# Performance work log

Measured on AMD Instinct MI355X. Metric: run time of the kernel, lower is better.

## Reference

```python
import jax, jax.numpy as jnp
import numpy as np

DIL = (1, 2, 4)      # dilation_rates
SEG = (512, 512, 512)  # segment_sizes
H = 16               # num_heads
D = 1024             # d_model
B, L = 2, 8192


def _mha(x, Wqkv, bqkv, Wo, bo):
    # x: [..., S, D]; standard self-attention (FlashMHA math)
    lead = x.shape[:-2]
    S = x.shape[-2]
    hd = D // H
    qkv = x @ Wqkv.T + bqkv                      # [..., S, 3D]
    q, k, v = jnp.split(qkv, 3, axis=-1)
    q = q.reshape(*lead, S, H, hd)
    k = k.reshape(*lead, S, H, hd)
    v = v.reshape(*lead, S, H, hd)
    scale = 1.0 / np.float32(np.sqrt(hd))
    scores = jnp.einsum('...qhd,...khd->...hqk', q, k) * scale
    a = jax.nn.softmax(scores, axis=-1)
    o = jnp.einsum('...hqk,...khd->...qhd', a, v).reshape(*lead, S, D)
    return o @ Wo.T + bo


def setup_inputs() -> dict:
    key = jax.random.key(0)
    ks = jax.random.split(key, 5)
    n = len(DIL)
    x = jax.random.normal(ks[0], (B, L, D), dtype=jnp.float32)
    Wqkv = 0.02 * jax.random.normal(ks[1], (n, 3 * D, D), dtype=jnp.float32)
    bqkv = jnp.zeros((n, 3 * D), dtype=jnp.float32)
    Wout = 0.02 * jax.random.normal(ks[2], (n, D, D), dtype=jnp.float32)
    bout = jnp.zeros((n, D), dtype=jnp.float32)
    return {"x": x, "Wqkv": Wqkv, "bqkv": bqkv, "Wout": Wout, "bout": bout}


def reference(x, Wqkv, bqkv, Wout, bout):
    b_, L_, D_ = x.shape
    n = len(DIL)
    # Faithful to the original: zip(weights, all_head_outputs) truncates to the
    # first n = len(dilation_rates) of the (branch, offset) outputs.
    pairs = [(br, off) for br in range(n) for off in range(DIL[br])][:n]
    outs = []
    for br, off in pairs:
        r, S = DIL[br], SEG[br]
        xs = x[:, off::r, :].reshape(b_, -1, S, D_)   # [B, n_seg, S, D]
        att = _mha(xs, Wqkv[br], bqkv[br], Wout[br], bout[br])
        full = jnp.zeros_like(x).at[:, off::r, :].set(att.reshape(b_, -1, D_))
        outs.append(full)
    w = jax.nn.softmax(jnp.full((n,), 1.0 / n, dtype=x.dtype))  # uniform -> 1/n each
    res = outs[0] * w[0]
    for i in range(1, n):
        res = res + w[i] * outs[i]
    return res
```

## Files before the change

### kernel.cpp

```cpp
#include <hip/hip_runtime.h>
#include <math.h>

#define TOK    16384
#define DMODEL 1024
#define H3     3072
#define QKD    2048
#define LSEQ   8192
#define CHUNK  8192

typedef unsigned short ushort_t;
using bf16x8 = __attribute__((ext_vector_type(8))) __bf16;
using us8    = __attribute__((ext_vector_type(8))) unsigned short;
using f32x4  = __attribute__((ext_vector_type(4))) float;

__device__ __forceinline__ unsigned short f2bf(float f) {
    unsigned int u = __float_as_uint(f);
    u += 0x7FFF + ((u >> 16) & 1);
    return (unsigned short)(u >> 16);
}
__device__ __forceinline__ float bf2f(unsigned short b) {
    return __uint_as_float(((unsigned int)b) << 16);
}
__device__ __forceinline__ bf16x8 us8_to_bf(us8 u) {
    union { us8 u; bf16x8 b; } t; t.u = u; return t.b;
}

__device__ __forceinline__ void gld16(const void* g, void* l) {
    __builtin_amdgcn_global_load_lds(
        (const __attribute__((address_space(1))) unsigned int*)g,
        (__attribute__((address_space(3))) unsigned int*)l, 16, 0, 0);
}

__global__ __launch_bounds__(256) void split_f32(
    const float* __restrict__ s, ushort_t* __restrict__ h,
    ushort_t* __restrict__ l, int n4, int perm)
{
    int i = blockIdx.x * 256 + threadIdx.x;
    if (i >= n4) return;
    int src = i;
    if (perm) {
        int row = i >> 8, col = i & 255;
        int chunk = row >> 13, p = row & 8191;
        int orow = (chunk << 13) + ((p & 4095) * 2 + (p >> 12));
        src = orow * 256 + col;
    }
    float4 v = ((const float4*)s)[src];
    ushort4 hp, lp;
    hp.x = f2bf(v.x); lp.x = f2bf(v.x - bf2f(hp.x));
    hp.y = f2bf(v.y); lp.y = f2bf(v.y - bf2f(hp.y));
    hp.z = f2bf(v.z); lp.z = f2bf(v.z - bf2f(hp.z));
    hp.w = f2bf(v.w); lp.w = f2bf(v.w - bf2f(hp.w));
    ((ushort4*)h)[i] = hp;
    ((ushort4*)l)[i] = lp;
}

__global__ __launch_bounds__(256) void gemm_split_nt(
    const ushort_t* __restrict__ Ah, const ushort_t* __restrict__ Al,
    const ushort_t* __restrict__ Wh, const ushort_t* __restrict__ Wl,
    const float* __restrict__ bias, float* __restrict__ C,
    ushort_t* __restrict__ Ch, ushort_t* __restrict__ Cl,
    ushort_t* __restrict__ Vth, ushort_t* __restrict__ Vtl,
    int M, int N, int K, float scale, int beta, int qkv_mode)
{
    __shared__ __align__(16) ushort_t As[2][8 * 512];
    __shared__ __align__(16) ushort_t Bs[2][8 * 512];

    const int tid  = threadIdx.x;
    const int lane = tid & 63;
    const int w    = tid >> 6;
    const int m0 = blockIdx.y * 128;
    const int n0 = blockIdx.x * 128;

    const bool isA = (w < 2);
    const int  fb  = (w & 1) * 4;
    const int  blk0 = isA ? m0 : n0;
    long soff[4];
#pragma unroll
    for (int i = 0; i < 4; ++i) {
        int row = blk0 + (fb + i) * 16 + (lane & 15);
        soff[i] = (long)row * K + (lane >> 4) * 8;
    }
    ushort_t* dst_h = (isA ? As[0] : Bs[0]) + fb * 512;
    ushort_t* dst_l = (isA ? As[1] : Bs[1]) + fb * 512;
    const ushort_t* src_h = isA ? Ah : Wh;
    const ushort_t* src_l = isA ? Al : Wl;

    const int am0 = (w >> 1) * 4;
    const int bn0 = (w & 1) * 4;

    f32x4 acc[4][4];
#pragma unroll
    for (int i = 0; i < 4; ++i)
#pragma unroll
        for (int j = 0; j < 4; ++j) acc[i][j] = (f32x4){0.f, 0.f, 0.f, 0.f};

    for (int k0 = 0; k0 < K; k0 += 32) {
#pragma unroll
        for (int i = 0; i < 4; ++i) {
            gld16(src_h + soff[i] + k0, dst_h + i * 512);
            gld16(src_l + soff[i] + k0, dst_l + i * 512);
        }
        __syncthreads();

        bf16x8 ah[4], al[4], bh[4], bl[4];
#pragma unroll
        for (int i = 0; i < 4; ++i) {
            ah[i] = *(const bf16x8*)(As[0] + (am0 + i) * 512 + lane * 8);
            al[i] = *(const bf16x8*)(As[1] + (am0 + i) * 512 + lane * 8);
            bh[i] = *(const bf16x8*)(Bs[0] + (bn0 + i) * 512 + lane * 8);
            bl[i] = *(const bf16x8*)(Bs[1] + (bn0 + i) * 512 + lane * 8);
        }
#pragma unroll
        for (int i = 0; i < 4; ++i)
#pragma unroll
            for (int j = 0; j < 4; ++j)
                acc[i][j] = __builtin_amdgcn_mfma_f32_16x16x32_bf16(
                    ah[i], bh[j], acc[i][j], 0, 0, 0);
#pragma unroll
        for (int i = 0; i < 4; ++i)
#pragma unroll
            for (int j = 0; j < 4; ++j)
                acc[i][j] = __builtin_amdgcn_mfma_f32_16x16x32_bf16(
                    al[i], bh[j], acc[i][j], 0, 0, 0);
#pragma unroll
        for (int i = 0; i < 4; ++i)
#pragma unroll
            for (int j = 0; j < 4; ++j)
                acc[i][j] = __builtin_amdgcn_mfma_f32_16x16x32_bf16(
                    ah[i], bl[j], acc[i][j], 0, 0, 0);
        __syncthreads();
    }

    const int wm = (w >> 1) * 64, wn = (w & 1) * 64;
    const int r0 = (lane >> 4) * 4;
    const int cn = lane & 15;

    if (qkv_mode) {
        const bool isV = (n0 >= 1024 * 2);
#pragma unroll
        for (int j = 0; j < 4; ++j) {
            int col = n0 + wn + j * 16 + cn;
            float bv = bias[col];
#pragma unroll
            for (int i = 0; i < 4; ++i) {
                int rowb = m0 + wm + i * 16 + r0;
                if (isV) {
                    unsigned short ha[4], la[4];
#pragma unroll
                    for (int r = 0; r < 4; ++r) {
                        float v = acc[i][j][r] + bv;
                        ha[r] = f2bf(v);
                        la[r] = f2bf(v - bf2f(ha[r]));
                    }
                    size_t vidx = (size_t)(col - 2048) * M + rowb;
                    *(ushort4*)(Vth + vidx) = make_ushort4(ha[0], ha[1], ha[2], ha[3]);
                    *(ushort4*)(Vtl + vidx) = make_ushort4(la[0], la[1], la[2], la[3]);
                } else {
#pragma unroll
                    for (int r = 0; r < 4; ++r) {
                        float v = acc[i][j][r] + bv;
                        unsigned short hb = f2bf(v);
                        size_t idx = (size_t)(rowb + r) * QKD + col;
                        Ch[idx] = hb;
                        Cl[idx] = f2bf(v - bf2f(hb));
                    }
                }
            }
        }
    } else {
#pragma unroll
        for (int j = 0; j < 4; ++j) {
            int col = n0 + wn + j * 16 + cn;
            float bv = bias[col];
#pragma unroll
            for (int i = 0; i < 4; ++i) {
                int rowb = m0 + wm + i * 16 + r0;
#pragma unroll
                for (int r = 0; r < 4; ++r) {
                    size_t idx = (size_t)(rowb + r) * N + col;
                    float v = scale * (acc[i][j][r] + bv);
                    C[idx] = beta ? (C[idx] + v) : v;
                }
            }
        }
    }
}

__global__ __launch_bounds__(256) void attn_mfma(
    const ushort_t* __restrict__ qkh, const ushort_t* __restrict__ qkl,
    const ushort_t* __restrict__ vth, const ushort_t* __restrict__ vtl,
    ushort_t* __restrict__ aoh, ushort_t* __restrict__ aol,
    int perm, long tok0)
{
    __shared__ __align__(16) ushort_t Kls[2][4096];
    __shared__ __align__(16) ushort_t Vls[2][4096];
    __shared__ __align__(16) float    Ps[4][16 * 68];

    const int tid  = threadIdx.x;
    const int lane = tid & 63;
    const int w    = tid >> 6;
    const int l15  = lane & 15;
    const int lg   = lane >> 4;
    const int qt = blockIdx.x, h = blockIdx.y, z = blockIdx.z;
    const int base = z * 512;

    bf16x8 qh[2], ql[2];
    {
        const int qrow = base + qt * 64 + w * 16 + l15;
        const size_t rb = (size_t)qrow * QKD + h * 64 + lg * 8;
        qh[0] = *(const bf16x8*)(qkh + rb);
        ql[0] = *(const bf16x8*)(qkl + rb);
        qh[1] = *(const bf16x8*)(qkh + rb + 32);
        ql[1] = *(const bf16x8*)(qkl + rb + 32);
    }

    const bool isV = (w >> 1) != 0;
    const int  jm  = (w & 1) * 2;
    const ushort_t* srcH = isV ? vth : qkh;
    const ushort_t* srcL = isV ? vtl : qkl;
    size_t so[4];
    ushort_t *dH[4], *dL[4];
#pragma unroll
    for (int dj = 0; dj < 2; ++dj)
#pragma unroll
        for (int ks = 0; ks < 2; ++ks) {
            const int j = jm + dj, idx = dj * 2 + ks;
            if (!isV)
                so[idx] = (size_t)(base + 16 * j + l15) * QKD + 1024 + h * 64 + 32 * ks + lg * 8;
            else
                so[idx] = (size_t)(h * 64 + 16 * j + l15) * CHUNK + base + 32 * ks + lg * 8;
            dH[idx] = (isV ? Vls[0] : Kls[0]) + (j * 2 + ks) * 512;
            dL[idx] = (isV ? Vls[1] : Kls[1]) + (j * 2 + ks) * 512;
        }
    const size_t kstep = isV ? 64 : (size_t)64 * QKD;

    f32x4 oacc[4];
#pragma unroll
    for (int j = 0; j < 4; ++j) oacc[j] = (f32x4){0.f, 0.f, 0.f, 0.f};
    float m_r[4] = {-INFINITY, -INFINITY, -INFINITY, -INFINITY};
    float l_r[4] = {0.f, 0.f, 0.f, 0.f};
    float* const pw = Ps[w];

    for (int kt = 0; kt < 8; ++kt) {
#pragma unroll
        for (int i = 0; i < 4; ++i) {
            gld16(srcH + so[i], dH[i]);
            gld16(srcL + so[i], dL[i]);
            so[i] += kstep;
        }
        __syncthreads();

        f32x4 s[4];
#pragma unroll
        for (int j = 0; j < 4; ++j) s[j] = (f32x4){0.f, 0.f, 0.f, 0.f};
#pragma unroll
        for (int j = 0; j < 4; ++j)
#pragma unroll
            for (int ks = 0; ks < 2; ++ks) {
                const bf16x8 kh = *(const bf16x8*)(&Kls[0][(j * 2 + ks) * 512 + lane * 8]);
                const bf16x8 kl = *(const bf16x8*)(&Kls[1][(j * 2 + ks) * 512 + lane * 8]);
                s[j] = __builtin_amdgcn_mfma_f32_16x16x32_bf16(qh[ks], kh, s[j], 0, 0, 0);
                s[j] = __builtin_amdgcn_mfma_f32_16x16x32_bf16(ql[ks], kh, s[j], 0, 0, 0);
                s[j] = __builtin_amdgcn_mfma_f32_16x16x32_bf16(qh[ks], kl, s[j], 0, 0, 0);
            }

        float alpha[4];
#pragma unroll
        for (int r = 0; r < 4; ++r) {
            float v = fmaxf(fmaxf(s[0][r], s[1][r]), fmaxf(s[2][r], s[3][r]));
            v = fmaxf(v, __shfl_xor(v, 1));
            v = fmaxf(v, __shfl_xor(v, 2));
            v = fmaxf(v, __shfl_xor(v, 4));
            v = fmaxf(v, __shfl_xor(v, 8));
            const float mn = fmaxf(m_r[r], 0.125f * v);
            alpha[r] = __expf(m_r[r] - mn);
            m_r[r] = mn;
            float sum = 0.f;
#pragma unroll
            for (int j = 0; j < 4; ++j) {
                const float p = __expf(fmaf(0.125f, s[j][r], -mn));
                s[j][r] = p;
                sum += p;
            }
            sum += __shfl_xor(sum, 1);
            sum += __shfl_xor(sum, 2);
            sum += __shfl_xor(sum, 4);
            sum += __shfl_xor(sum, 8);
            l_r[r] = l_r[r] * alpha[r] + sum;
        }

#pragma unroll
        for (int r = 0; r < 4; ++r)
#pragma unroll
            for (int j = 0; j < 4; ++j)
                pw[(lg * 4 + r) * 68 + 16 * j + l15] = s[j][r];
        asm volatile("s_waitcnt lgkmcnt(0)" ::: "memory");
        __builtin_amdgcn_sched_barrier(0);

#pragma unroll
        for (int j = 0; j < 4; ++j)
#pragma unroll
            for (int r = 0; r < 4; ++r) oacc[j][r] *= alpha[r];

#pragma unroll
        for (int ks = 0; ks < 2; ++ks) {
            const float* pp = pw + l15 * 68 + ks * 32 + lg * 8;
            const float4 pa = *(const float4*)pp;
            const float4 pb = *(const float4*)(pp + 4);
            const float pf[8] = {pa.x, pa.y, pa.z, pa.w, pb.x, pb.y, pb.z, pb.w};
            us8 hu, lu;
#pragma unroll
            for (int e = 0; e < 8; ++e) {
                const unsigned short hb = f2bf(pf[e]);
                hu[e] = hb;
                lu[e] = f2bf(pf[e] - bf2f(hb));
            }
            const bf16x8 ph = us8_to_bf(hu);
            const bf16x8 pl = us8_to_bf(lu);
#pragma unroll
            for (int j = 0; j < 4; ++j) {
                const bf16x8 vh = *(const bf16x8*)(&Vls[0][(j * 2 + ks) * 512 + lane * 8]);
                const bf16x8 vl = *(const bf16x8*)(&Vls[1][(j * 2 + ks) * 512 + lane * 8]);
                oacc[j] = __builtin_amdgcn_mfma_f32_16x16x32_bf16(ph, vh, oacc[j], 0, 0, 0);
                oacc[j] = __builtin_amdgcn_mfma_f32_16x16x32_bf16(pl, vh, oacc[j], 0, 0, 0);
                oacc[j] = __builtin_amdgcn_mfma_f32_16x16x32_bf16(ph, vl, oacc[j], 0, 0, 0);
            }
        }
        __syncthreads();
    }

    float linv[4];
#pragma unroll
    for (int r = 0; r < 4; ++r) linv[r] = 1.f / l_r[r];
#pragma unroll
    for (int j = 0; j < 4; ++j)
#pragma unroll
        for (int r = 0; r < 4; ++r)
            pw[(lg * 4 + r) * 68 + 16 * j + l15] = oacc[j][r] * linv[r];
    asm volatile("s_waitcnt lgkmcnt(0)" ::: "memory");
    __builtin_amdgcn_sched_barrier(0);

    {
        const int rr = lane >> 2, c0 = (lane & 3) * 16;
        const float* rp = pw + rr * 68 + c0;
        const int p_local = base + qt * 64 + w * 16 + rr;
        const long tok = tok0 + (perm ? (long)((p_local & 4095) * 2 + (p_local >> 12))
                                      : (long)p_local);
        const size_t off = (size_t)tok * DMODEL + h * 64 + c0;
        const float4 f0 = *(const float4*)rp;
        const float4 f1 = *(const float4*)(rp + 4);
        const float4 f2 = *(const float4*)(rp + 8);
        const float4 f3 = *(const float4*)(rp + 12);
        const float ff[16] = {f0.x, f0.y, f0.z, f0.w, f1.x, f1.y, f1.z, f1.w,
                              f2.x, f2.y, f2.z, f2.w, f3.x, f3.y, f3.z, f3.w};
        us8 h0, h1, l0, l1;
#pragma unroll
        for (int e = 0; e < 8; ++e) {
            unsigned short hb = f2bf(ff[e]);
            h0[e] = hb; l0[e] = f2bf(ff[e] - bf2f(hb));
            hb = f2bf(ff[e + 8]);
            h1[e] = hb; l1[e] = f2bf(ff[e + 8] - bf2f(hb));
        }
        *(us8*)(aoh + off)     = h0;
        *(us8*)(aoh + off + 8) = h1;
        *(us8*)(aol + off)     = l0;
        *(us8*)(aol + off + 8) = l1;
    }
}

extern "C" void kernel_launch(void* const* d_in, const int* in_sizes, int n_in,
                              void* d_out, int out_size, void* d_ws, size_t ws_size,
                              hipStream_t stream) {
    const float* x    = (const float*)d_in[0];
    const float* Wqkv = (const float*)d_in[1];
    const float* bqkv = (const float*)d_in[2];
    const float* Wout = (const float*)d_in[3];
    const float* bout = (const float*)d_in[4];
    float* out = (float*)d_out;

    char* wp = (char*)d_ws;
    ushort_t* xh  = (ushort_t*)wp; wp += (size_t)TOK * DMODEL * 2;
    ushort_t* xl  = (ushort_t*)wp; wp += (size_t)TOK * DMODEL * 2;
    ushort_t* wqh = (ushort_t*)wp; wp += (size_t)H3 * DMODEL * 2;
    ushort_t* wql = (ushort_t*)wp; wp += (size_t)H3 * DMODEL * 2;
    ushort_t* woh = (ushort_t*)wp; wp += (size_t)DMODEL * DMODEL * 2;
    ushort_t* wol = (ushort_t*)wp; wp += (size_t)DMODEL * DMODEL * 2;
    ushort_t* qkh = (ushort_t*)wp; wp += (size_t)CHUNK * QKD * 2;
    ushort_t* qkl = (ushort_t*)wp; wp += (size_t)CHUNK * QKD * 2;
    ushort_t* vth = (ushort_t*)wp; wp += (size_t)DMODEL * CHUNK * 2;
    ushort_t* vtl = (ushort_t*)wp; wp += (size_t)DMODEL * CHUNK * 2;
    ushort_t* aoh = (ushort_t*)wp; wp += (size_t)TOK * DMODEL * 2;
    ushort_t* aol = (ushort_t*)wp;

    dim3 blk(256);
    const float third = 1.0f / 3.0f;

    for (int br = 0; br < 2; ++br) {
        {
            int n4x = TOK * DMODEL / 4;
            split_f32<<<(n4x + 255) / 256, blk, 0, stream>>>(x, xh, xl, n4x, br);
            int n4q = H3 * DMODEL / 4;
            split_f32<<<(n4q + 255) / 256, blk, 0, stream>>>(
                Wqkv + (size_t)br * H3 * DMODEL, wqh, wql, n4q, 0);
            int n4o = DMODEL * DMODEL / 4;
            split_f32<<<(n4o + 255) / 256, blk, 0, stream>>>(
                Wout + (size_t)br * DMODEL * DMODEL, woh, wol, n4o, 0);
        }
        for (int c = 0; c < TOK / CHUNK; ++c) {
            gemm_split_nt<<<dim3(H3 / 128, CHUNK / 128), blk, 0, stream>>>(
                xh + (size_t)c * CHUNK * DMODEL, xl + (size_t)c * CHUNK * DMODEL,
                wqh, wql, bqkv + (size_t)br * H3, nullptr,
                qkh, qkl, vth, vtl,
                CHUNK, H3, DMODEL, 1.0f, 0, 1);
            attn_mfma<<<dim3(8, 16, 16), blk, 0, stream>>>(
                qkh, qkl, vth, vtl, aoh, aol, br, (long)c * CHUNK);
        }
        gemm_split_nt<<<dim3(DMODEL / 128, TOK / 128), blk, 0, stream>>>(
            aoh, aol, woh, wol, bout + (size_t)br * DMODEL, out,
            nullptr, nullptr, nullptr, nullptr,
            TOK, DMODEL, DMODEL, third, br, 0);
    }
}
```

Before: 1.724 ms.

## Move row permutation into GEMM epilogue, register-prefetch B, and swizzle block order

The x split now runs once instead of once per branch. The row permutation for branch 1 moves from the input split into the QKV GEMM epilogue, which now writes Q/K rows and V-transposed columns to permuted positions. The GEMM no longer stages the weight tile through shared memory. Each wave loads its B fragments straight from global memory into registers and double-buffers them across a K step of 64, while only A goes through LDS. The change also adds an XCD-aware block-index swizzle and launch_bounds with min 3 blocks per CU, trading extra global traffic for B and scattered epilogue stores for less LDS use and better overlap.

```diff
diff --git a/kernel.cpp b/kernel.cpp
--- a/kernel.cpp
+++ b/kernel.cpp
@@ -33,18 +33,11 @@
 
 __global__ __launch_bounds__(256) void split_f32(
     const float* __restrict__ s, ushort_t* __restrict__ h,
-    ushort_t* __restrict__ l, int n4, int perm)
+    ushort_t* __restrict__ l, int n4)
 {
     int i = blockIdx.x * 256 + threadIdx.x;
     if (i >= n4) return;
-    int src = i;
-    if (perm) {
-        int row = i >> 8, col = i & 255;
-        int chunk = row >> 13, p = row & 8191;
-        int orow = (chunk << 13) + ((p & 4095) * 2 + (p >> 12));
-        src = orow * 256 + col;
-    }
-    float4 v = ((const float4*)s)[src];
+    float4 v = ((const float4*)s)[i];
     ushort4 hp, lp;
     hp.x = f2bf(v.x); lp.x = f2bf(v.x - bf2f(hp.x));
     hp.y = f2bf(v.y); lp.y = f2bf(v.y - bf2f(hp.y));
@@ -54,39 +47,46 @@
     ((ushort4*)l)[i] = lp;
 }
 
-__global__ __launch_bounds__(256) void gemm_split_nt(
+__global__ __launch_bounds__(256, 3) void gemm_split_nt(
     const ushort_t* __restrict__ Ah, const ushort_t* __restrict__ Al,
     const ushort_t* __restrict__ Wh, const ushort_t* __restrict__ Wl,
     const float* __restrict__ bias, float* __restrict__ C,
     ushort_t* __restrict__ Ch, ushort_t* __restrict__ Cl,
     ushort_t* __restrict__ Vth, ushort_t* __restrict__ Vtl,
-    int M, int N, int K, float scale, int beta, int qkv_mode)
+    int M, int N, int K, float scale, int beta, int qkv_mode, int perm)
 {
     __shared__ __align__(16) ushort_t As[2][8 * 512];
-    __shared__ __align__(16) ushort_t Bs[2][8 * 512];
 
     const int tid  = threadIdx.x;
     const int lane = tid & 63;
     const int w    = tid >> 6;
-    const int m0 = blockIdx.y * 128;
-    const int n0 = blockIdx.x * 128;
-
-    const bool isA = (w < 2);
-    const int  fb  = (w & 1) * 4;
-    const int  blk0 = isA ? m0 : n0;
-    long soff[4];
-#pragma unroll
-    for (int i = 0; i < 4; ++i) {
-        int row = blk0 + (fb + i) * 16 + (lane & 15);
-        soff[i] = (long)row * K + (lane >> 4) * 8;
-    }
-    ushort_t* dst_h = (isA ? As[0] : Bs[0]) + fb * 512;
-    ushort_t* dst_l = (isA ? As[1] : Bs[1]) + fb * 512;
-    const ushort_t* src_h = isA ? Ah : Wh;
-    const ushort_t* src_l = isA ? Al : Wl;
+
+    const int nwg = gridDim.x * gridDim.y;
+    const int id  = blockIdx.y * gridDim.x + blockIdx.x;
+    const int gci = (id & 7) * (nwg >> 3) + (id >> 3);
+    const int bx  = gci / gridDim.y;
+    const int by  = gci % gridDim.y;
+    const int m0 = by * 128;
+    const int n0 = bx * 128;
+
+    int soA[2];
+#pragma unroll
+    for (int i = 0; i < 2; ++i) {
+        int row = m0 + (w * 2 + i) * 16 + (lane & 15);
+        soA[i] = row * K + (lane >> 4) * 8;
+    }
+    ushort_t* dAh = As[0] + (w * 2) * 512;
+    ushort_t* dAl = As[1] + (w * 2) * 512;
+
+    const int bn0 = (w & 1) * 4;
+    int soB[4];
+#pragma unroll
+    for (int j = 0; j < 4; ++j) {
+        int row = n0 + (bn0 + j) * 16 + (lane & 15);
+        soB[j] = row * K + (lane >> 4) * 8;
+    }
 
     const int am0 = (w >> 1) * 4;
-    const int bn0 = (w & 1) * 4;
 
     f32x4 acc[4][4];
 #pragma unroll
@@ -94,49 +94,74 @@
 #pragma unroll
         for (int j = 0; j < 4; ++j) acc[i][j] = (f32x4){0.f, 0.f, 0.f, 0.f};
 
-    for (int k0 = 0; k0 < K; k0 += 32) {
-#pragma unroll
-        for (int i = 0; i < 4; ++i) {
-            gld16(src_h + soff[i] + k0, dst_h + i * 512);
-            gld16(src_l + soff[i] + k0, dst_l + i * 512);
-        }
-        __syncthreads();
-
-        bf16x8 ah[4], al[4], bh[4], bl[4];
-#pragma unroll
-        for (int i = 0; i < 4; ++i) {
-            ah[i] = *(const bf16x8*)(As[0] + (am0 + i) * 512 + lane * 8);
-            al[i] = *(const bf16x8*)(As[1] + (am0 + i) * 512 + lane * 8);
-            bh[i] = *(const bf16x8*)(Bs[0] + (bn0 + i) * 512 + lane * 8);
-            bl[i] = *(const bf16x8*)(Bs[1] + (bn0 + i) * 512 + lane * 8);
-        }
-#pragma unroll
-        for (int i = 0; i < 4; ++i)
-#pragma unroll
-            for (int j = 0; j < 4; ++j)
-                acc[i][j] = __builtin_amdgcn_mfma_f32_16x16x32_bf16(
-                    ah[i], bh[j], acc[i][j], 0, 0, 0);
-#pragma unroll
-        for (int i = 0; i < 4; ++i)
-#pragma unroll
-            for (int j = 0; j < 4; ++j)
-                acc[i][j] = __builtin_amdgcn_mfma_f32_16x16x32_bf16(
-                    al[i], bh[j], acc[i][j], 0, 0, 0);
-#pragma unroll
-        for (int i = 0; i < 4; ++i)
-#pragma unroll
-            for (int j = 0; j < 4; ++j)
-                acc[i][j] = __builtin_amdgcn_mfma_f32_16x16x32_bf16(
-                    ah[i], bl[j], acc[i][j], 0, 0, 0);
-        __syncthreads();
-    }
+    bf16x8 b0h[4], b0l[4], b1h[4], b1l[4];
+#pragma unroll
+    for (int j = 0; j < 4; ++j) {
+        b0h[j] = *(const bf16x8*)(Wh + soB[j]);
+        b0l[j] = *(const bf16x8*)(Wl + soB[j]);
+    }
+
+#define STAGE_A(k0)                                                      \
+    {                                                                    \
+        _Pragma("unroll")                                                \
+        for (int i = 0; i < 2; ++i) {                                    \
+            gld16(Ah + soA[i] + (k0), dAh + i * 512);                    \
+            gld16(Al + soA[i] + (k0), dAl + i * 512);                    \
+        }                                                                \
+    }
+
+#define MFMA_BLOCK(BH, BL)                                               \
+    {                                                                    \
+        _Pragma("unroll")                                                \
+        for (int i = 0; i < 4; ++i) {                                    \
+            const bf16x8 ah = *(const bf16x8*)(As[0] + (am0 + i) * 512 + lane * 8); \
+            const bf16x8 al = *(const bf16x8*)(As[1] + (am0 + i) * 512 + lane * 8); \
+            _Pragma("unroll")                                            \
+            for (int j = 0; j < 4; ++j)                                  \
+                acc[i][j] = __builtin_amdgcn_mfma_f32_16x16x32_bf16(     \
+                    ah, BH[j], acc[i][j], 0, 0, 0);                      \
+            _Pragma("unroll")                                            \
+            for (int j = 0; j < 4; ++j)                                  \
+                acc[i][j] = __builtin_amdgcn_mfma_f32_16x16x32_bf16(     \
+                    al, BH[j], acc[i][j], 0, 0, 0);                      \
+            _Pragma("unroll")                                            \
+            for (int j = 0; j < 4; ++j)                                  \
+                acc[i][j] = __builtin_amdgcn_mfma_f32_16x16x32_bf16(     \
+                    ah, BL[j], acc[i][j], 0, 0, 0);                      \
+        }                                                                \
+    }
+
+    for (int k0 = 0; k0 < K; k0 += 64) {
+        STAGE_A(k0);
+        __syncthreads();
+#pragma unroll
+        for (int j = 0; j < 4; ++j) {
+            b1h[j] = *(const bf16x8*)(Wh + soB[j] + k0 + 32);
+            b1l[j] = *(const bf16x8*)(Wl + soB[j] + k0 + 32);
+        }
+        MFMA_BLOCK(b0h, b0l);
+        __syncthreads();
+        STAGE_A(k0 + 32);
+        __syncthreads();
+        if (k0 + 64 < K) {
+#pragma unroll
+            for (int j = 0; j < 4; ++j) {
+                b0h[j] = *(const bf16x8*)(Wh + soB[j] + k0 + 64);
+                b0l[j] = *(const bf16x8*)(Wl + soB[j] + k0 + 64);
+            }
+        }
+        MFMA_BLOCK(b1h, b1l);
+        __syncthreads();
+    }
+#undef STAGE_A
+#undef MFMA_BLOCK
 
     const int wm = (w >> 1) * 64, wn = (w & 1) * 64;
     const int r0 = (lane >> 4) * 4;
     const int cn = lane & 15;
 
     if (qkv_mode) {
-        const bool isV = (n0 >= 1024 * 2);
+        const bool isV = (n0 >= 2048);
 #pragma unroll
         for (int j = 0; j < 4; ++j) {
             int col = n0 + wn + j * 16 + cn;
@@ -152,15 +177,25 @@
                         ha[r] = f2bf(v);
                         la[r] = f2bf(v - bf2f(ha[r]));
                     }
-                    size_t vidx = (size_t)(col - 2048) * M + rowb;
-                    *(ushort4*)(Vth + vidx) = make_ushort4(ha[0], ha[1], ha[2], ha[3]);
-                    *(ushort4*)(Vtl + vidx) = make_ushort4(la[0], la[1], la[2], la[3]);
+                    size_t vb = (size_t)(col - 2048) * M;
+                    if (perm) {
+                        int hhf = rowb >> 1;
+                        *(ushort2*)(Vth + vb + hhf)        = make_ushort2(ha[0], ha[2]);
+                        *(ushort2*)(Vth + vb + 4096 + hhf) = make_ushort2(ha[1], ha[3]);
+                        *(ushort2*)(Vtl + vb + hhf)        = make_ushort2(la[0], la[2]);
+                        *(ushort2*)(Vtl + vb + 4096 + hhf) = make_ushort2(la[1], la[3]);
+                    } else {
+                        *(ushort4*)(Vth + vb + rowb) = make_ushort4(ha[0], ha[1], ha[2], ha[3]);
+                        *(ushort4*)(Vtl + vb + rowb) = make_ushort4(la[0], la[1], la[2], la[3]);
+                    }
                 } else {
 #pragma unroll
                     for (int r = 0; r < 4; ++r) {
                         float v = acc[i][j][r] + bv;
                         unsigned short hb = f2bf(v);
-                        size_t idx = (size_t)(rowb + r) * QKD + col;
+                        int orow = rowb + r;
+                        int prow = perm ? ((orow & 1) * 4096 + (orow >> 1)) : orow;
+                        size_t idx = (size_t)prow * QKD + col;
                         Ch[idx] = hb;
                         Cl[idx] = f2bf(v - bf2f(hb));
                     }
@@ -395,29 +430,32 @@
     dim3 blk(256);
     const float third = 1.0f / 3.0f;
 
+    {
+        int n4x = TOK * DMODEL / 4;
+        split_f32<<<(n4x + 255) / 256, blk, 0, stream>>>(x, xh, xl, n4x);
+    }
+
     for (int br = 0; br < 2; ++br) {
         {
-            int n4x = TOK * DMODEL / 4;
-            split_f32<<<(n4x + 255) / 256, blk, 0, stream>>>(x, xh, xl, n4x, br);
             int n4q = H3 * DMODEL / 4;
             split_f32<<<(n4q + 255) / 256, blk, 0, stream>>>(
-                Wqkv + (size_t)br * H3 * DMODEL, wqh, wql, n4q, 0);
+                Wqkv + (size_t)br * H3 * DMODEL, wqh, wql, n4q);
             int n4o = DMODEL * DMODEL / 4;
             split_f32<<<(n4o + 255) / 256, blk, 0, stream>>>(
-                Wout + (size_t)br * DMODEL * DMODEL, woh, wol, n4o, 0);
+                Wout + (size_t)br * DMODEL * DMODEL, woh, wol, n4o);
         }
         for (int c = 0; c < TOK / CHUNK; ++c) {
             gemm_split_nt<<<dim3(H3 / 128, CHUNK / 128), blk, 0, stream>>>(
                 xh + (size_t)c * CHUNK * DMODEL, xl + (size_t)c * CHUNK * DMODEL,
                 wqh, wql, bqkv + (size_t)br * H3, nullptr,
                 qkh, qkl, vth, vtl,
-                CHUNK, H3, DMODEL, 1.0f, 0, 1);
+                CHUNK, H3, DMODEL, 1.0f, 0, 1, br);
             attn_mfma<<<dim3(8, 16, 16), blk, 0, stream>>>(
                 qkh, qkl, vth, vtl, aoh, aol, br, (long)c * CHUNK);
         }
         gemm_split_nt<<<dim3(DMODEL / 128, TOK / 128), blk, 0, stream>>>(
             aoh, aol, woh, wol, bout + (size_t)br * DMODEL, out,
             nullptr, nullptr, nullptr, nullptr,
-            TOK, DMODEL, DMODEL, third, br, 0);
-    }
-}
+            TOK, DMODEL, DMODEL, third, br, 0, 0);
+    }
+}
```

Result: slower. 2.453 ms (+42.3%).

## Move dilation permutation into QKV GEMM epilogue and swizzle GEMM block order

Applied to the files above, without the earlier changes.

Instead of re-splitting x with a permuted gather for each branch, x is split into bf16 hi/lo pairs once, and the QKV GEMM writes Q/K rows and the transposed V to permuted (even/odd interleaved) positions in its epilogue. This drops one full split pass over x and its strided reads. A workgroup-ID swizzle is also added to the GEMM so that neighbouring blocks share tiles in cache. In exchange the V stores become 2-element writes instead of 4-element writes, and the Q/K scatter writes are less contiguous.

```diff
diff --git a/kernel.cpp b/kernel.cpp
--- a/kernel.cpp
+++ b/kernel.cpp
@@ -33,18 +33,11 @@
 
 __global__ __launch_bounds__(256) void split_f32(
     const float* __restrict__ s, ushort_t* __restrict__ h,
-    ushort_t* __restrict__ l, int n4, int perm)
+    ushort_t* __restrict__ l, int n4)
 {
     int i = blockIdx.x * 256 + threadIdx.x;
     if (i >= n4) return;
-    int src = i;
-    if (perm) {
-        int row = i >> 8, col = i & 255;
-        int chunk = row >> 13, p = row & 8191;
-        int orow = (chunk << 13) + ((p & 4095) * 2 + (p >> 12));
-        src = orow * 256 + col;
-    }
-    float4 v = ((const float4*)s)[src];
+    float4 v = ((const float4*)s)[i];
     ushort4 hp, lp;
     hp.x = f2bf(v.x); lp.x = f2bf(v.x - bf2f(hp.x));
     hp.y = f2bf(v.y); lp.y = f2bf(v.y - bf2f(hp.y));
@@ -60,7 +53,7 @@
     const float* __restrict__ bias, float* __restrict__ C,
     ushort_t* __restrict__ Ch, ushort_t* __restrict__ Cl,
     ushort_t* __restrict__ Vth, ushort_t* __restrict__ Vtl,
-    int M, int N, int K, float scale, int beta, int qkv_mode)
+    int M, int N, int K, float scale, int beta, int qkv_mode, int perm)
 {
     __shared__ __align__(16) ushort_t As[2][8 * 512];
     __shared__ __align__(16) ushort_t Bs[2][8 * 512];
@@ -68,8 +61,14 @@
     const int tid  = threadIdx.x;
     const int lane = tid & 63;
     const int w    = tid >> 6;
-    const int m0 = blockIdx.y * 128;
-    const int n0 = blockIdx.x * 128;
+
+    const int nwg = gridDim.x * gridDim.y;
+    const int id  = blockIdx.y * gridDim.x + blockIdx.x;
+    const int swz = (id & 7) * (nwg >> 3) + (id >> 3);
+    const int bx  = swz % gridDim.x;
+    const int by  = swz / gridDim.x;
+    const int m0 = by * 128;
+    const int n0 = bx * 128;
 
     const bool isA = (w < 2);
     const int  fb  = (w & 1) * 4;
@@ -136,7 +135,7 @@
     const int cn = lane & 15;
 
     if (qkv_mode) {
-        const bool isV = (n0 >= 1024 * 2);
+        const bool isV = (n0 >= 2048);
 #pragma unroll
         for (int j = 0; j < 4; ++j) {
             int col = n0 + wn + j * 16 + cn;
@@ -152,15 +151,25 @@
                         ha[r] = f2bf(v);
                         la[r] = f2bf(v - bf2f(ha[r]));
                     }
-                    size_t vidx = (size_t)(col - 2048) * M + rowb;
-                    *(ushort4*)(Vth + vidx) = make_ushort4(ha[0], ha[1], ha[2], ha[3]);
-                    *(ushort4*)(Vtl + vidx) = make_ushort4(la[0], la[1], la[2], la[3]);
+                    size_t vb = (size_t)(col - 2048) * M;
+                    if (perm) {
+                        int hhf = rowb >> 1;
+                        *(ushort2*)(Vth + vb + hhf)        = make_ushort2(ha[0], ha[2]);
+                        *(ushort2*)(Vth + vb + 4096 + hhf) = make_ushort2(ha[1], ha[3]);
+                        *(ushort2*)(Vtl + vb + hhf)        = make_ushort2(la[0], la[2]);
+                        *(ushort2*)(Vtl + vb + 4096 + hhf) = make_ushort2(la[1], la[3]);
+                    } else {
+                        *(ushort4*)(Vth + vb + rowb) = make_ushort4(ha[0], ha[1], ha[2], ha[3]);
+                        *(ushort4*)(Vtl + vb + rowb) = make_ushort4(la[0], la[1], la[2], la[3]);
+                    }
                 } else {
 #pragma unroll
                     for (int r = 0; r < 4; ++r) {
                         float v = acc[i][j][r] + bv;
                         unsigned short hb = f2bf(v);
-                        size_t idx = (size_t)(rowb + r) * QKD + col;
+                        int orow = rowb + r;
+                        int prow = perm ? ((orow & 1) * 4096 + (orow >> 1)) : orow;
+                        size_t idx = (size_t)prow * QKD + col;
                         Ch[idx] = hb;
                         Cl[idx] = f2bf(v - bf2f(hb));
                     }
@@ -395,29 +404,32 @@
     dim3 blk(256);
     const float third = 1.0f / 3.0f;
 
+    {
+        int n4x = TOK * DMODEL / 4;
+        split_f32<<<(n4x + 255) / 256, blk, 0, stream>>>(x, xh, xl, n4x);
+    }
+
     for (int br = 0; br < 2; ++br) {
         {
-            int n4x = TOK * DMODEL / 4;
-            split_f32<<<(n4x + 255) / 256, blk, 0, stream>>>(x, xh, xl, n4x, br);
             int n4q = H3 * DMODEL / 4;
             split_f32<<<(n4q + 255) / 256, blk, 0, stream>>>(
-                Wqkv + (size_t)br * H3 * DMODEL, wqh, wql, n4q, 0);
+                Wqkv + (size_t)br * H3 * DMODEL, wqh, wql, n4q);
             int n4o = DMODEL * DMODEL / 4;
             split_f32<<<(n4o + 255) / 256, blk, 0, stream>>>(
-                Wout + (size_t)br * DMODEL * DMODEL, woh, wol, n4o, 0);
+                Wout + (size_t)br * DMODEL * DMODEL, woh, wol, n4o);
         }
         for (int c = 0; c < TOK / CHUNK; ++c) {
             gemm_split_nt<<<dim3(H3 / 128, CHUNK / 128), blk, 0, stream>>>(
                 xh + (size_t)c * CHUNK * DMODEL, xl + (size_t)c * CHUNK * DMODEL,
                 wqh, wql, bqkv + (size_t)br * H3, nullptr,
                 qkh, qkl, vth, vtl,
-                CHUNK, H3, DMODEL, 1.0f, 0, 1);
+                CHUNK, H3, DMODEL, 1.0f, 0, 1, br);
             attn_mfma<<<dim3(8, 16, 16), blk, 0, stream>>>(
                 qkh, qkl, vth, vtl, aoh, aol, br, (long)c * CHUNK);
         }
         gemm_split_nt<<<dim3(DMODEL / 128, TOK / 128), blk, 0, stream>>>(
             aoh, aol, woh, wol, bout + (size_t)br * DMODEL, out,
             nullptr, nullptr, nullptr, nullptr,
-            TOK, DMODEL, DMODEL, third, br, 0);
-    }
-}
+            TOK, DMODEL, DMODEL, third, br, 0, 0);
+    }
+}
```

Measured after the change: 1.736 ms. Within noise of the previous version (+0.7%).
